# Performance work log

Hardware: AMD Instinct MI355X
Metric: run time of the kernel (lower is better)

## Reference

```python
import jax, jax.numpy as jnp
from jax import lax
import numpy as np

STEP = 0.01
BS = 32  # blocksize


def conv(x, w, b=None, stride=1, pad=0):
    y = lax.conv_general_dilated(x, w, (stride, stride), [(pad, pad), (pad, pad)],
                                 dimension_numbers=('NCHW', 'OIHW', 'NCHW'))
    if b is not None:
        y = y + b[None, :, None, None]
    return y


def prelu(x, a):
    return jnp.where(x >= 0, x, a * x)


def depth_to_space(x, bs):
    # matches Reshape_Concat_Adap: each [C] pixel vector viewed as (C', bs, bs)
    B, C, h, w = x.shape
    C2 = C // (bs * bs)
    y = x.reshape(B, C2, bs, bs, h, w)
    y = y.transpose(0, 1, 4, 2, 5, 3)  # B, C2, h, bs, w, bs
    return y.reshape(B, C2, h * bs, w * bs)


def setup_inputs() -> dict:
    key = jax.random.key(0)
    ks = jax.random.split(key, 32)

    def W(k, shape):
        fan_in = shape[1] * shape[2] * shape[3]
        return (jax.random.normal(k, shape, jnp.float32) * np.sqrt(2.0 / fan_in)).astype(jnp.float32)

    inp = {
        'x': jax.random.normal(ks[0], (4, 1, 192, 192), jnp.float32),
        'epoch': 1,
        'd1_w': W(ks[1], (16, 1, 4, 4)),
        'd2_w': W(ks[2], (256, 16, 4, 4)),
        'd3_w': W(ks[3], (1024, 256, 2, 2)),
        'd4_w': W(ks[4], (154, 1024, 1, 1)),
        'q1_w': W(ks[5], (154, 154, 1, 1)), 'q1_b': jnp.zeros((154,), jnp.float32),
        'q2_w': W(ks[6], (154, 154, 1, 1)), 'q2_b': jnp.zeros((154,), jnp.float32),
        'q3_w': W(ks[7], (154, 154, 1, 1)), 'q3_b': jnp.zeros((154,), jnp.float32),
        'up_w': W(ks[8], (1024, 154, 1, 1)), 'up_b': jnp.zeros((1024,), jnp.float32),
        'c1_w': W(ks[9], (64, 1, 3, 3)), 'c1_b': jnp.zeros((64,), jnp.float32), 'c1_a': jnp.float32(0.25),
        'c2_w': W(ks[10], (64, 64, 3, 3)), 'c2_b': jnp.zeros((64,), jnp.float32), 'c2_a': jnp.float32(0.25),
        'c3_w': W(ks[11], (64, 64, 3, 3)), 'c3_b': jnp.zeros((64,), jnp.float32), 'c3_a': jnp.float32(0.25),
        'c4_w': W(ks[12], (64, 64, 3, 3)), 'c4_b': jnp.zeros((64,), jnp.float32), 'c4_a': jnp.float32(0.25),
        'c5_w': W(ks[13], (256, 64, 3, 3)), 'c5_b': jnp.zeros((256,), jnp.float32),
    }
    return inp


def reference(x, epoch, d1_w, d2_w, d3_w, d4_w, q1_w, q1_b, q2_w, q2_b, q3_w, q3_b,
              up_w, up_b, c1_w, c1_b, c1_a, c2_w, c2_b, c2_a, c3_w, c3_b, c3_a,
              c4_w, c4_b, c4_a, c5_w, c5_b):
    step = jnp.float32(STEP)
    relu = jax.nn.relu
    # down path
    h = relu(conv(x, d1_w, stride=4))
    h = relu(conv(h, d2_w, stride=4))
    h = relu(conv(h, d3_w, stride=2))
    x4 = conv(h, d4_w)                      # [B,154,H/32,W/32]
    # STE quantize + dequantize
    q = x4 + lax.stop_gradient(jnp.floor(x4 / step) - x4)
    xr = q * step
    t = xr
    t = relu(conv(t, q1_w, q1_b)) + t
    t = relu(conv(t, q2_w, q2_b)) + t
    t = relu(conv(t, q3_w, q3_b)) + t
    x_comp = t + xr
    # upsample to blocksize^2 channels, then depth-to-space
    u = conv(x_comp, up_w, up_b)            # [B,1024,H/32,W/32]
    y = depth_to_space(u, BS)               # [B,1,H,W]
    # refinement CNN
    b1 = prelu(conv(y, c1_w, c1_b, pad=1), c1_a)
    b2 = prelu(conv(b1 + y, c2_w, c2_b, pad=1), c2_a)
    b3 = prelu(conv(b2 + b1, c3_w, c3_b, pad=1), c3_a)
    b4 = prelu(conv(b3 + b2, c4_w, c4_b, pad=1), c4_a)
    b5 = conv(b4 + b3, c5_w, c5_b, pad=1)   # [B,256,H,W]
    B, _, H, Wd = b5.shape
    return (b5.reshape(B, 1, 256, H, Wd), x_comp, x4)
```

## Files before the change

### kernel.cpp

```cpp
#include <hip/hip_runtime.h>
#include <math.h>

#define N_B 4
#define IMG 192
#define P 194

typedef __attribute__((ext_vector_type(8))) short short8;
typedef __attribute__((ext_vector_type(4))) float f32x4;

__device__ __forceinline__ unsigned f2bf(float f) {
  unsigned u = __float_as_uint(f);
  return (u + 0x7fffu + ((u >> 16) & 1u)) >> 16;
}
__device__ __forceinline__ float bf2f(unsigned b) {
  return __uint_as_float(b << 16);
}
__device__ __forceinline__ int swz(int pix) {
  return (pix & 7) << 4;
}
__device__ __forceinline__ void gload_lds16(const void* g, void* l) {
  __builtin_amdgcn_global_load_lds(
      (const __attribute__((address_space(1))) void*)g,
      (__attribute__((address_space(3))) void*)l, 16, 0, 0);
}

__global__ void k_d1(const float* __restrict__ x, const float* __restrict__ w,
                     float* __restrict__ out) {
  int idx = blockIdx.x * 256 + threadIdx.x;
  if (idx >= N_B * 16 * 48 * 48) return;
  int xq = idx % 48; int t = idx / 48; int yq = t % 48; t /= 48;
  int oc = t % 16; int b = t / 16;
  const float* xp = x + (b * IMG + yq * 4) * IMG + xq * 4;
  const float* wp = w + oc * 16;
  float s = 0.f;
#pragma unroll
  for (int dy = 0; dy < 4; ++dy)
#pragma unroll
    for (int dx = 0; dx < 4; ++dx)
      s = fmaf(xp[dy * IMG + dx], wp[dy * 4 + dx], s);
  out[idx] = fmaxf(s, 0.f);
}

__global__ void k_d2(const float* __restrict__ h1, const float* __restrict__ d2t,
                     float* __restrict__ out) {
  int idx = blockIdx.x * 256 + threadIdx.x;
  if (idx >= N_B * 144 * 256) return;
  int oc = idx & 255; int t = idx >> 8; int p = t % 144; int b = t / 144;
  int yq = p / 12, xq = p % 12;
  float s = 0.f;
  for (int ci = 0; ci < 16; ++ci) {
    const float* ip = h1 + ((b * 16 + ci) * 48 + yq * 4) * 48 + xq * 4;
    const float* wp = d2t + (ci * 16) * 256 + oc;
#pragma unroll
    for (int dy = 0; dy < 4; ++dy)
#pragma unroll
      for (int dx = 0; dx < 4; ++dx)
        s = fmaf(ip[dy * 48 + dx], wp[(dy * 4 + dx) * 256], s);
  }
  out[((size_t)b * 144 + p) * 256 + oc] = fmaxf(s, 0.f);
}

__global__ __launch_bounds__(256) void k_d3(const float* __restrict__ h2t,
                                            const float* __restrict__ w3p,
                                            float* __restrict__ out) {
  int idx = blockIdx.x * 256 + threadIdx.x;
  if (idx >= N_B * 36 * 1024) return;
  int oc = idx & 1023; int t = idx >> 10; int p6 = t % 36; int b = t / 36;
  int yq = p6 / 6, xq = p6 % 6;
  const float* p00 = h2t + ((size_t)b * 144 + (2 * yq) * 12 + 2 * xq) * 256;
  const float* p01 = p00 + 256;
  const float* p10 = p00 + 12 * 256;
  const float* p11 = p10 + 256;
  const float* w0 = w3p + oc;
  float a0 = 0.f, a1 = 0.f, a2 = 0.f, a3 = 0.f;
  for (int ci = 0; ci < 256; ++ci) {
    a0 = fmaf(p00[ci], w0[(size_t)(0 * 256 + ci) * 1024], a0);
    a1 = fmaf(p01[ci], w0[(size_t)(1 * 256 + ci) * 1024], a1);
    a2 = fmaf(p10[ci], w0[(size_t)(2 * 256 + ci) * 1024], a2);
    a3 = fmaf(p11[ci], w0[(size_t)(3 * 256 + ci) * 1024], a3);
  }
  out[((size_t)b * 36 + p6) * 1024 + oc] = fmaxf((a0 + a1) + (a2 + a3), 0.f);
}

__global__ __launch_bounds__(512) void k_mid(
    const float* __restrict__ h3t, const float* __restrict__ d4t,
    const float* __restrict__ qt, const float* __restrict__ q1_b,
    const float* __restrict__ q2_b, const float* __restrict__ q3_b,
    const float* __restrict__ upt, const float* __restrict__ up_b,
    float* __restrict__ x4_out, float* __restrict__ xcomp_out,
    float* __restrict__ y_out) {
  __shared__ float hv[1024];
  __shared__ float part[512];
  __shared__ float tv[160];
  __shared__ float xrv[160];
  int blk = blockIdx.x;
  int b = blk / 36, p = blk % 36;
  int tid = threadIdx.x;
  for (int i = tid; i < 1024; i += 512) hv[i] = h3t[(size_t)blk * 1024 + i];
  __syncthreads();
  {
    int half = tid >> 8, oc = tid & 255;
    float s = 0.f;
    if (oc < 154) {
      const float* wp = d4t + (size_t)half * 512 * 160 + oc;
      const float* hp = hv + half * 512;
      float a0 = 0.f, a1 = 0.f, a2 = 0.f, a3 = 0.f;
      for (int i = 0; i < 512; i += 4) {
        a0 = fmaf(hp[i], wp[(size_t)i * 160], a0);
        a1 = fmaf(hp[i + 1], wp[(size_t)(i + 1) * 160], a1);
        a2 = fmaf(hp[i + 2], wp[(size_t)(i + 2) * 160], a2);
        a3 = fmaf(hp[i + 3], wp[(size_t)(i + 3) * 160], a3);
      }
      s = (a0 + a1) + (a2 + a3);
    }
    part[tid] = s;
  }
  __syncthreads();
  if (tid < 154) {
    float s = part[tid] + part[tid + 256];
    x4_out[(b * 154 + tid) * 36 + p] = s;
    float q = floorf(s / 0.01f) * 0.01f;
    xrv[tid] = q;
    tv[tid] = q;
  }
  __syncthreads();
  const float* qb[3] = {q1_b, q2_b, q3_b};
  for (int l = 0; l < 3; ++l) {
    float s = 0.f;
    if (tid < 154) {
      const float* wp = qt + (size_t)l * 154 * 160 + tid;
      float a0 = 0.f, a1 = 0.f;
      int i = 0;
      for (; i + 1 < 154; i += 2) {
        a0 = fmaf(tv[i], wp[(size_t)i * 160], a0);
        a1 = fmaf(tv[i + 1], wp[(size_t)(i + 1) * 160], a1);
      }
      if (i < 154) a0 = fmaf(tv[i], wp[(size_t)i * 160], a0);
      s = qb[l][tid] + a0 + a1;
    }
    __syncthreads();
    if (tid < 154) tv[tid] = fmaxf(s, 0.f) + tv[tid];
    __syncthreads();
  }
  if (tid < 154) {
    float xc = tv[tid] + xrv[tid];
    tv[tid] = xc;
    xcomp_out[(b * 154 + tid) * 36 + p] = xc;
  }
  __syncthreads();
  int h = p / 6, w6 = p % 6;
#pragma unroll
  for (int k = 0; k < 2; ++k) {
    int co = k * 512 + tid;
    const float* wp = upt + co;
    float a0 = 0.f, a1 = 0.f;
    int i = 0;
    for (; i + 1 < 154; i += 2) {
      a0 = fmaf(tv[i], wp[(size_t)i * 1024], a0);
      a1 = fmaf(tv[i + 1], wp[(size_t)(i + 1) * 1024], a1);
    }
    if (i < 154) a0 = fmaf(tv[i], wp[(size_t)i * 1024], a0);
    float s = up_b[co] + a0 + a1;
    int i32 = co >> 5, j = co & 31;
    y_out[(b * IMG + h * 32 + i32) * IMG + w6 * 32 + j] = s;
  }
}

__global__ __launch_bounds__(256) void k_c1b(const float* __restrict__ y,
                                             const float* __restrict__ w,
                                             const float* __restrict__ bias,
                                             const float* __restrict__ a_p,
                                             short* __restrict__ B1,
                                             short* __restrict__ S1) {
  int idx = blockIdx.x * 256 + threadIdx.x;
  if (idx >= N_B * IMG * IMG) return;
  int X = idx % IMG; int t = idx / IMG; int Y = t % IMG; int b = t / IMG;
  float p[9];
#pragma unroll
  for (int dy = 0; dy < 3; ++dy)
#pragma unroll
    for (int dx = 0; dx < 3; ++dx) {
      int gy = Y + dy - 1, gx = X + dx - 1;
      p[dy * 3 + dx] = ((unsigned)gy < (unsigned)IMG && (unsigned)gx < (unsigned)IMG)
                           ? y[(b * IMG + gy) * IMG + gx]
                           : 0.f;
    }
  float a = *a_p;
  float yc = p[4];
  size_t base = (((size_t)b * P + Y + 1) * P + X + 1) * 64;
  for (int oc = 0; oc < 64; oc += 8) {
    unsigned bw[4], sw[4];
#pragma unroll
    for (int j = 0; j < 8; ++j) {
      float s = bias[oc + j];
      const float* wq = w + (oc + j) * 9;
#pragma unroll
      for (int k = 0; k < 9; ++k) s = fmaf(p[k], wq[k], s);
      s = s >= 0.f ? s : a * s;
      float sv = s + yc;
      if (j & 1) { bw[j >> 1] |= f2bf(s) << 16; sw[j >> 1] |= f2bf(sv) << 16; }
      else       { bw[j >> 1] = f2bf(s);        sw[j >> 1] = f2bf(sv); }
    }
    *(uint4*)(B1 + base + oc) = make_uint4(bw[0], bw[1], bw[2], bw[3]);
    *(uint4*)(S1 + base + oc) = make_uint4(sw[0], sw[1], sw[2], sw[3]);
  }
}

#define WPA (64 * 64 * 9)
#define WPB (256 * 64 * 9)
#define WD3N (4 * 256 * 1024)
#define RINGN (4 * 4 * 772 * 8)
#define D4TN (1024 * 154)
#define QTN (3 * 154 * 154)
#define UPTN (154 * 1024)
#define D2TN (256 * 16 * 16)
#define PREPN (3 * WPA + WPB + WD3N + RINGN + D4TN + QTN + UPTN + D2TN)
__global__ __launch_bounds__(256) void k_prep(
    const float* __restrict__ w2, const float* __restrict__ w3,
    const float* __restrict__ w4, const float* __restrict__ w5,
    const float* __restrict__ d3w, const float* __restrict__ d4w,
    const float* __restrict__ q1w, const float* __restrict__ q2w,
    const float* __restrict__ q3w, const float* __restrict__ upw,
    const float* __restrict__ d2w,
    short* __restrict__ o2, short* __restrict__ o3,
    short* __restrict__ o4, short* __restrict__ o5,
    float* __restrict__ w3p, float* __restrict__ d4t,
    float* __restrict__ qt, float* __restrict__ upt,
    float* __restrict__ d2t,
    short* __restrict__ s0, short* __restrict__ s1,
    short* __restrict__ s2, short* __restrict__ s3) {
  int idx = blockIdx.x * 256 + threadIdx.x;
  if (idx < 3 * WPA + WPB) {
    int which, id;
    if (idx < WPA) { which = 0; id = idx; }
    else if (idx < 2 * WPA) { which = 1; id = idx - WPA; }
    else if (idx < 3 * WPA) { which = 2; id = idx - 2 * WPA; }
    else { which = 3; id = idx - 3 * WPA; }
    const float* w = (which == 0) ? w2 : (which == 1) ? w3 : (which == 2) ? w4 : w5;
    short* o = (which == 0) ? o2 : (which == 1) ? o3 : (which == 2) ? o4 : o5;
    int OC = (which == 3) ? 256 : 64;
    int ic = id & 63; int t = id >> 6; int r = t % OC; int tap = t / OC;
    int oc = (which < 3) ? (((r >> 2) & 3) * 16 + ((r >> 4) & 3) * 4 + (r & 3)) : r;
    int ks = ic >> 5, lg = (ic >> 3) & 3, j = ic & 7, li = r & 15, ocblk = r >> 4;
    size_t dst = ((size_t)(tap * 2 + ks) * (OC >> 4) + ocblk) * 512 +
                 (lg * 16 + li) * 8 + j;
    o[dst] = (short)f2bf(w[((size_t)oc * 64 + ic) * 9 + tap]);
    return;
  }
  idx -= 3 * WPA + WPB;
  if (idx < WD3N) {
    int oc = idx & 1023; int ci = (idx >> 10) & 255; int tap = idx >> 18;
    w3p[idx] = d3w[((size_t)oc * 256 + ci) * 4 + tap];
    return;
  }
  idx -= WD3N;
  if (idx < RINGN) {
    int chunk = idx & 7; int t = idx >> 3;
    int r = t % 772; t /= 772; int b = t % 4; int buf = t / 4;
    int y, x;
    if (r < 194) { y = 0; x = r; }
    else if (r < 388) { y = 193; x = r - 194; }
    else { int q = r - 388; y = 1 + (q >> 1); x = (q & 1) ? 193 : 0; }
    short* p = (buf == 0) ? s0 : (buf == 1) ? s1 : (buf == 2) ? s2 : s3;
    *(uint4*)(p + (((size_t)b * P + y) * P + x) * 64 + chunk * 8) =
        make_uint4(0u, 0u, 0u, 0u);
    return;
  }
  idx -= RINGN;
  if (idx < D4TN) {
    int oc = idx % 154; int ic = idx / 154;
    d4t[(size_t)ic * 160 + oc] = d4w[(size_t)oc * 1024 + ic];
    return;
  }
  idx -= D4TN;
  if (idx < QTN) {
    int l = idx / (154 * 154); int rem = idx % (154 * 154);
    int oc = rem % 154; int ic = rem / 154;
    const float* qw = (l == 0) ? q1w : (l == 1) ? q2w : q3w;
    qt[(size_t)l * 154 * 160 + (size_t)ic * 160 + oc] =
        qw[(size_t)oc * 154 + ic];
    return;
  }
  idx -= QTN;
  if (idx < UPTN) {
    int co = idx % 1024; int ic = idx / 1024;
    upt[(size_t)ic * 1024 + co] = upw[(size_t)co * 154 + ic];
    return;
  }
  idx -= UPTN;
  if (idx < D2TN) {
    int oc = idx & 255; int t = idx >> 8; int tap = t & 15; int ci = t >> 4;
    d2t[((size_t)ci * 16 + tap) * 256 + oc] =
        d2w[((size_t)oc * 16 + ci) * 16 + tap];
  }
}

template <int MODE>
__global__ __launch_bounds__(256) void k_conv3x3n(
    const short* __restrict__ sin, const short* __restrict__ bprev,
    const short* __restrict__ wbf, const float* __restrict__ bias,
    const float* __restrict__ a_p, short* __restrict__ bout,
    short* __restrict__ sout) {
  __shared__ __align__(16) char smem[300 * 128];
  int tid = threadIdx.x;
  int b = blockIdx.z;
  int x0 = blockIdx.x * 48, y0 = blockIdx.y * 4;
  int w = tid >> 6, lane = tid & 63, li = lane & 15, lg = lane >> 4;

  for (int c = w; c < 38; c += 4) {
    int o = c * 1024 + lane * 16;
    if (o < 300 * 128) {
      int pix = o >> 7;
      int icq = ((o >> 4) & 7) ^ (pix & 7);
      const short* src = sin +
          (((size_t)b * P + y0 + pix / 50) * P + x0 + pix % 50) * 64 + icq * 8;
      gload_lds16(src, smem + c * 1024);
    }
  }
  __syncthreads();

  const short* abase = wbf + (lane << 3);
  const int astride = 64 * 32;

  f32x4 acc[4][3];
#pragma unroll
  for (int mt = 0; mt < 4; ++mt)
#pragma unroll
    for (int nt = 0; nt < 3; ++nt) acc[mt][nt] = (f32x4){0.f, 0.f, 0.f, 0.f};

#define LOADA(s, dst)                                                          \
  {                                                                            \
    const short* p_ = abase + (size_t)(s) * astride;                           \
    _Pragma("unroll") for (int mt = 0; mt < 4; ++mt)                           \
        dst[mt] = *(const short8*)(p_ + mt * 512);                             \
  }
#define LOADB(s, dst)                                                          \
  {                                                                            \
    const int tap_ = (s) >> 1, ks_ = (s) & 1;                                  \
    const int dy_ = tap_ / 3, dx_ = tap_ % 3;                                  \
    _Pragma("unroll") for (int nt = 0; nt < 3; ++nt) {                         \
      int pix_ = (w + dy_) * 50 + nt * 16 + dx_ + li;                          \
      int byte_ = (pix_ * 128 + ks_ * 64 + lg * 16) ^ swz(pix_);               \
      dst[nt] = *(const short8*)(smem + byte_);                                \
    }                                                                          \
  }

  short8 Abuf[2][4];
  short8 Bbuf[3];
  LOADA(0, Abuf[0]);
#pragma unroll
  for (int s = 0; s < 18; ++s) {
    if (s + 1 < 18) LOADA(s + 1, Abuf[(s + 1) & 1]);
    LOADB(s, Bbuf);
    short8* Ac = Abuf[s & 1];
#pragma unroll
    for (int mt = 0; mt < 4; ++mt)
#pragma unroll
      for (int nt = 0; nt < 3; ++nt)
        acc[mt][nt] = __builtin_amdgcn_mfma_f32_16x16x32_bf16(Ac[mt], Bbuf[nt],
                                                              acc[mt][nt], 0, 0, 0);
  }
#undef LOADA
#undef LOADB

  float a = *a_p;
  int gy = y0 + w;
#pragma unroll
  for (int nt = 0; nt < 3; ++nt) {
    int gx = x0 + nt * 16 + li;
    float r[16];
#pragma unroll
    for (int mt = 0; mt < 4; ++mt) {
      float4 bv = *(const float4*)(bias + lg * 16 + mt * 4);
      f32x4 v = acc[mt][nt];
      float t0 = v[0] + bv.x, t1 = v[1] + bv.y, t2 = v[2] + bv.z, t3 = v[3] + bv.w;
      r[mt * 4 + 0] = t0 >= 0.f ? t0 : a * t0;
      r[mt * 4 + 1] = t1 >= 0.f ? t1 : a * t1;
      r[mt * 4 + 2] = t2 >= 0.f ? t2 : a * t2;
      r[mt * 4 + 3] = t3 >= 0.f ? t3 : a * t3;
    }
    size_t pi = (((size_t)b * P + gy + 1) * P + gx + 1) * 64 + lg * 16;
    if (MODE == 0) {
      uint4 u0 = make_uint4(f2bf(r[0]) | (f2bf(r[1]) << 16),
                            f2bf(r[2]) | (f2bf(r[3]) << 16),
                            f2bf(r[4]) | (f2bf(r[5]) << 16),
                            f2bf(r[6]) | (f2bf(r[7]) << 16));
      uint4 u1 = make_uint4(f2bf(r[8]) | (f2bf(r[9]) << 16),
                            f2bf(r[10]) | (f2bf(r[11]) << 16),
                            f2bf(r[12]) | (f2bf(r[13]) << 16),
                            f2bf(r[14]) | (f2bf(r[15]) << 16));
      *(uint4*)(bout + pi) = u0;
      *(uint4*)(bout + pi + 8) = u1;
    }
    uint4 p0 = *(const uint4*)(bprev + pi);
    uint4 p1 = *(const uint4*)(bprev + pi + 8);
    unsigned pw[8] = {p0.x, p0.y, p0.z, p0.w, p1.x, p1.y, p1.z, p1.w};
    unsigned so[8];
#pragma unroll
    for (int k = 0; k < 8; ++k) {
      float s0 = r[2 * k] + bf2f(pw[k] & 0xffffu);
      float s1 = r[2 * k + 1] + bf2f(pw[k] >> 16);
      so[k] = f2bf(s0) | (f2bf(s1) << 16);
    }
    *(uint4*)(sout + pi) = make_uint4(so[0], so[1], so[2], so[3]);
    *(uint4*)(sout + pi + 8) = make_uint4(so[4], so[5], so[6], so[7]);
  }
}

__global__ __launch_bounds__(256) void k_conv5n(
    const short* __restrict__ sin, const short* __restrict__ wbf,
    const float* __restrict__ bias, float* __restrict__ fout) {
  __shared__ __align__(16) char smem[300 * 128];
  int tid = threadIdx.x;
  int g = blockIdx.z & 3, b = blockIdx.z >> 2;
  int x0 = blockIdx.x * 48, y0 = blockIdx.y * 4;
  int w = tid >> 6, lane = tid & 63, li = lane & 15, lg = lane >> 4;

  for (int c = w; c < 38; c += 4) {
    int o = c * 1024 + lane * 16;
    if (o < 300 * 128) {
      int pix = o >> 7;
      int icq = ((o >> 4) & 7) ^ (pix & 7);
      const short* src = sin +
          (((size_t)b * P + y0 + pix / 50) * P + x0 + pix % 50) * 64 + icq * 8;
      gload_lds16(src, smem + c * 1024);
    }
  }
  __syncthreads();

  const short* abase = wbf + (size_t)(g << 2) * 512 + (lane << 3);
  const int astride = 256 * 32;

  f32x4 acc[4][3];
#pragma unroll
  for (int mt = 0; mt < 4; ++mt)
#pragma unroll
    for (int nt = 0; nt < 3; ++nt) acc[mt][nt] = (f32x4){0.f, 0.f, 0.f, 0.f};

#define LOADA5(s, dst)                                                         \
  {                                                                            \
    const short* p_ = abase + (size_t)(s) * astride;                           \
    _Pragma("unroll") for (int mt = 0; mt < 4; ++mt)                           \
        dst[mt] = *(const short8*)(p_ + mt * 512);                             \
  }
#define LOADB5(s, dst)                                                         \
  {                                                                            \
    const int tap_ = (s) >> 1, ks_ = (s) & 1;                                  \
    const int dy_ = tap_ / 3, dx_ = tap_ % 3;                                  \
    _Pragma("unroll") for (int nt = 0; nt < 3; ++nt) {                         \
      int pix_ = (w + dy_) * 50 + nt * 16 + dx_ + li;                          \
      int byte_ = (pix_ * 128 + ks_ * 64 + lg * 16) ^ swz(pix_);               \
      dst[nt] = *(const short8*)(smem + byte_);                                \
    }                                                                          \
  }

  short8 Abuf[2][4];
  short8 Bbuf[3];
  LOADA5(0, Abuf[0]);
#pragma unroll
  for (int s = 0; s < 18; ++s) {
    if (s + 1 < 18) LOADA5(s + 1, Abuf[(s + 1) & 1]);
    LOADB5(s, Bbuf);
    short8* Ac = Abuf[s & 1];
#pragma unroll
    for (int mt = 0; mt < 4; ++mt)
#pragma unroll
      for (int nt = 0; nt < 3; ++nt)
        acc[mt][nt] = __builtin_amdgcn_mfma_f32_16x16x32_bf16(Bbuf[nt], Ac[mt],
                                                              acc[mt][nt], 0, 0, 0);
  }
#undef LOADA5
#undef LOADB5

  int gy = y0 + w;
#pragma unroll
  for (int nt = 0; nt < 3; ++nt) {
    int gx = x0 + nt * 16 + lg * 4;
#pragma unroll
    for (int mt = 0; mt < 4; ++mt) {
      int oc = g * 64 + mt * 16 + li;
      float bv = bias[oc];
      f32x4 v = acc[mt][nt];
      *(float4*)(fout + (((size_t)b * 256 + oc) * IMG + gy) * IMG + gx) =
          make_float4(v[0] + bv, v[1] + bv, v[2] + bv, v[3] + bv);
    }
  }
}

extern "C" void kernel_launch(void* const* d_in, const int* in_sizes, int n_in,
                              void* d_out, int out_size, void* d_ws, size_t ws_size,
                              hipStream_t stream) {
  const float* x    = (const float*)d_in[0];
  const float* d1_w = (const float*)d_in[2];
  const float* d2_w = (const float*)d_in[3];
  const float* d3_w = (const float*)d_in[4];
  const float* d4_w = (const float*)d_in[5];
  const float* q1_w = (const float*)d_in[6];
  const float* q1_b = (const float*)d_in[7];
  const float* q2_w = (const float*)d_in[8];
  const float* q2_b = (const float*)d_in[9];
  const float* q3_w = (const float*)d_in[10];
  const float* q3_b = (const float*)d_in[11];
  const float* up_w = (const float*)d_in[12];
  const float* up_b = (const float*)d_in[13];
  const float* c1_w = (const float*)d_in[14];
  const float* c1_b = (const float*)d_in[15];
  const float* c1_a = (const float*)d_in[16];
  const float* c2_w = (const float*)d_in[17];
  const float* c2_b = (const float*)d_in[18];
  const float* c2_a = (const float*)d_in[19];
  const float* c3_w = (const float*)d_in[20];
  const float* c3_b = (const float*)d_in[21];
  const float* c3_a = (const float*)d_in[22];
  const float* c4_w = (const float*)d_in[23];
  const float* c4_b = (const float*)d_in[24];
  const float* c4_a = (const float*)d_in[25];
  const float* c5_w = (const float*)d_in[26];
  const float* c5_b = (const float*)d_in[27];

  float* out = (float*)d_out;
  float* ws  = (float*)d_ws;

  const size_t B5  = (size_t)N_B * 256 * IMG * IMG;
  const size_t SML = (size_t)N_B * 154 * 36;
  float* out_b5    = out;
  float* out_xcomp = out + B5;
  float* out_x4    = out + B5 + SML;

  const size_t PADBUF = (size_t)N_B * P * P * 64 / 2;
  size_t off = 0;
  float* h1   = ws + off; off += (size_t)N_B * 16 * 48 * 48;
  float* h2t  = ws + off; off += (size_t)N_B * 144 * 256;
  float* h3t  = ws + off; off += (size_t)N_B * 36 * 1024;
  float* w3p  = ws + off; off += (size_t)4 * 256 * 1024;
  float* d4t  = ws + off; off += (size_t)1024 * 160;
  float* qt   = ws + off; off += (size_t)3 * 154 * 160;
  float* upt  = ws + off; off += (size_t)154 * 1024;
  float* d2t  = ws + off; off += (size_t)256 * 16 * 16;
  float* ybuf = ws + off; off += (size_t)N_B * IMG * IMG;
  short* sl0  = (short*)(ws + off); off += PADBUF;
  short* sl1  = (short*)(ws + off); off += PADBUF;
  short* sl2  = (short*)(ws + off); off += PADBUF;
  short* sl3  = (short*)(ws + off); off += PADBUF;
  short* wb2  = (short*)(ws + off); off += 9 * 64 * 64 / 2;
  short* wb3  = (short*)(ws + off); off += 9 * 64 * 64 / 2;
  short* wb4  = (short*)(ws + off); off += 9 * 64 * 64 / 2;
  short* wb5  = (short*)(ws + off); off += 9 * 256 * 64 / 2;

  k_prep<<<(PREPN + 255) / 256, 256, 0, stream>>>(
      c2_w, c3_w, c4_w, c5_w, d3_w, d4_w, q1_w, q2_w, q3_w, up_w, d2_w,
      wb2, wb3, wb4, wb5, w3p, d4t, qt, upt, d2t, sl0, sl1, sl2, sl3);

  k_d1<<<(N_B * 16 * 48 * 48 + 255) / 256, 256, 0, stream>>>(x, d1_w, h1);
  k_d2<<<(N_B * 144 * 256 + 255) / 256, 256, 0, stream>>>(h1, d2t, h2t);
  k_d3<<<(N_B * 36 * 1024 + 255) / 256, 256, 0, stream>>>(h2t, w3p, h3t);

  k_mid<<<N_B * 36, 512, 0, stream>>>(h3t, d4t, qt, q1_b, q2_b, q3_b,
                                      upt, up_b, out_x4, out_xcomp, ybuf);

  k_c1b<<<(N_B * IMG * IMG + 255) / 256, 256, 0, stream>>>(ybuf, c1_w, c1_b, c1_a,
                                                           sl1 , sl0 );

  dim3 cg(4, 48, N_B);
  k_conv3x3n<0><<<cg, 256, 0, stream>>>(sl0, sl1, wb2, c2_b, c2_a, sl2, sl3);
  k_conv3x3n<0><<<cg, 256, 0, stream>>>(sl3, sl2, wb3, c3_b, c3_a, sl1, sl0);
  k_conv3x3n<1><<<cg, 256, 0, stream>>>(sl0, sl1, wb4, c4_b, c4_a, nullptr, sl3);
  dim3 cg5(4, 48, N_B * 4);
  k_conv5n<<<cg5, 256, 0, stream>>>(sl3, wb5, c5_b, out_b5);
}
```

Baseline: 285.3 us.

## Register-block d3 over four pixels and reuse conv5 input tile across two OC groups

k_d3 now computes four output pixels per thread, so each weight load is reused four times, and the grid shrinks to 144 blocks. The w3p prep loop is rewritten to read d3w sequentially and scatter writes, giving coalesced reads instead of coalesced writes. k_conv5n processes two 64-channel output groups per block, so the LDS input tile is loaded once for 128 channels and the grid halves. The cost is fewer blocks, which lowers parallelism, and each conv5 block now runs two sequential MFMA passes.

```diff
diff --git a/kernel.cpp b/kernel.cpp
--- a/kernel.cpp
+++ b/kernel.cpp
@@ -63,23 +63,39 @@
 __global__ __launch_bounds__(256) void k_d3(const float* __restrict__ h2t,
                                             const float* __restrict__ w3p,
                                             float* __restrict__ out) {
-  int idx = blockIdx.x * 256 + threadIdx.x;
-  if (idx >= N_B * 36 * 1024) return;
-  int oc = idx & 1023; int t = idx >> 10; int p6 = t % 36; int b = t / 36;
-  int yq = p6 / 6, xq = p6 % 6;
-  const float* p00 = h2t + ((size_t)b * 144 + (2 * yq) * 12 + 2 * xq) * 256;
-  const float* p01 = p00 + 256;
-  const float* p10 = p00 + 12 * 256;
-  const float* p11 = p10 + 256;
+  int tid = threadIdx.x;
+  int blk = blockIdx.x;
+  int og = blk & 3; int t = blk >> 2; int pg = t % 9; int b = t / 9;
+  int oc = og * 256 + tid;
   const float* w0 = w3p + oc;
-  float a0 = 0.f, a1 = 0.f, a2 = 0.f, a3 = 0.f;
+  const float* base[4];
+#pragma unroll
+  for (int k = 0; k < 4; ++k) {
+    int p6 = pg * 4 + k;
+    int yq = p6 / 6, xq = p6 % 6;
+    base[k] = h2t + ((size_t)b * 144 + (2 * yq) * 12 + 2 * xq) * 256;
+  }
+  float a0[4] = {0, 0, 0, 0}, a1[4] = {0, 0, 0, 0};
+  float a2[4] = {0, 0, 0, 0}, a3[4] = {0, 0, 0, 0};
   for (int ci = 0; ci < 256; ++ci) {
-    a0 = fmaf(p00[ci], w0[(size_t)(0 * 256 + ci) * 1024], a0);
-    a1 = fmaf(p01[ci], w0[(size_t)(1 * 256 + ci) * 1024], a1);
-    a2 = fmaf(p10[ci], w0[(size_t)(2 * 256 + ci) * 1024], a2);
-    a3 = fmaf(p11[ci], w0[(size_t)(3 * 256 + ci) * 1024], a3);
-  }
-  out[((size_t)b * 36 + p6) * 1024 + oc] = fmaxf((a0 + a1) + (a2 + a3), 0.f);
+    float w0v = w0[(size_t)(0 * 256 + ci) * 1024];
+    float w1v = w0[(size_t)(1 * 256 + ci) * 1024];
+    float w2v = w0[(size_t)(2 * 256 + ci) * 1024];
+    float w3v = w0[(size_t)(3 * 256 + ci) * 1024];
+#pragma unroll
+    for (int k = 0; k < 4; ++k) {
+      a0[k] = fmaf(base[k][ci], w0v, a0[k]);
+      a1[k] = fmaf(base[k][256 + ci], w1v, a1[k]);
+      a2[k] = fmaf(base[k][12 * 256 + ci], w2v, a2[k]);
+      a3[k] = fmaf(base[k][12 * 256 + 256 + ci], w3v, a3[k]);
+    }
+  }
+#pragma unroll
+  for (int k = 0; k < 4; ++k) {
+    int p6 = pg * 4 + k;
+    out[((size_t)b * 36 + p6) * 1024 + oc] =
+        fmaxf((a0[k] + a1[k]) + (a2[k] + a3[k]), 0.f);
+  }
 }
 
 __global__ __launch_bounds__(512) void k_mid(
@@ -249,8 +265,8 @@
   }
   idx -= 3 * WPA + WPB;
   if (idx < WD3N) {
-    int oc = idx & 1023; int ci = (idx >> 10) & 255; int tap = idx >> 18;
-    w3p[idx] = d3w[((size_t)oc * 256 + ci) * 4 + tap];
+    int tap = idx & 3; int ci = (idx >> 2) & 255; int oc = idx >> 10;
+    w3p[((size_t)tap * 256 + ci) * 1024 + oc] = d3w[idx];
     return;
   }
   idx -= WD3N;
@@ -412,7 +428,7 @@
     const float* __restrict__ bias, float* __restrict__ fout) {
   __shared__ __align__(16) char smem[300 * 128];
   int tid = threadIdx.x;
-  int g = blockIdx.z & 3, b = blockIdx.z >> 2;
+  int gh = blockIdx.z & 1, b = blockIdx.z >> 1;
   int x0 = blockIdx.x * 48, y0 = blockIdx.y * 4;
   int w = tid >> 6, lane = tid & 63, li = lane & 15, lg = lane >> 4;
 
@@ -428,18 +444,12 @@
   }
   __syncthreads();
 
-  const short* abase = wbf + (size_t)(g << 2) * 512 + (lane << 3);
   const int astride = 256 * 32;
-
-  f32x4 acc[4][3];
-#pragma unroll
-  for (int mt = 0; mt < 4; ++mt)
-#pragma unroll
-    for (int nt = 0; nt < 3; ++nt) acc[mt][nt] = (f32x4){0.f, 0.f, 0.f, 0.f};
-
-#define LOADA5(s, dst)                                                         \
+  int gy = y0 + w;
+
+#define LOADA5(s, dst, ab)                                                     \
   {                                                                            \
-    const short* p_ = abase + (size_t)(s) * astride;                           \
+    const short* p_ = (ab) + (size_t)(s) * astride;                            \
     _Pragma("unroll") for (int mt = 0; mt < 4; ++mt)                           \
         dst[mt] = *(const short8*)(p_ + mt * 512);                             \
   }
@@ -454,37 +464,48 @@
     }                                                                          \
   }
 
-  short8 Abuf[2][4];
-  short8 Bbuf[3];
-  LOADA5(0, Abuf[0]);
-#pragma unroll
-  for (int s = 0; s < 18; ++s) {
-    if (s + 1 < 18) LOADA5(s + 1, Abuf[(s + 1) & 1]);
-    LOADB5(s, Bbuf);
-    short8* Ac = Abuf[s & 1];
+#pragma unroll
+  for (int gg = 0; gg < 2; ++gg) {
+    const int g = gh * 2 + gg;
+    const short* abase = wbf + (size_t)(g << 2) * 512 + (lane << 3);
+
+    f32x4 acc[4][3];
 #pragma unroll
     for (int mt = 0; mt < 4; ++mt)
 #pragma unroll
-      for (int nt = 0; nt < 3; ++nt)
-        acc[mt][nt] = __builtin_amdgcn_mfma_f32_16x16x32_bf16(Bbuf[nt], Ac[mt],
-                                                              acc[mt][nt], 0, 0, 0);
+      for (int nt = 0; nt < 3; ++nt) acc[mt][nt] = (f32x4){0.f, 0.f, 0.f, 0.f};
+
+    short8 Abuf[2][4];
+    short8 Bbuf[3];
+    LOADA5(0, Abuf[0], abase);
+#pragma unroll
+    for (int s = 0; s < 18; ++s) {
+      if (s + 1 < 18) LOADA5(s + 1, Abuf[(s + 1) & 1], abase);
+      LOADB5(s, Bbuf);
+      short8* Ac = Abuf[s & 1];
+#pragma unroll
+      for (int mt = 0; mt < 4; ++mt)
+#pragma unroll
+        for (int nt = 0; nt < 3; ++nt)
+          acc[mt][nt] = __builtin_amdgcn_mfma_f32_16x16x32_bf16(
+              Bbuf[nt], Ac[mt], acc[mt][nt], 0, 0, 0);
+    }
+
+#pragma unroll
+    for (int nt = 0; nt < 3; ++nt) {
+      int gx = x0 + nt * 16 + lg * 4;
+#pragma unroll
+      for (int mt = 0; mt < 4; ++mt) {
+        int oc = g * 64 + mt * 16 + li;
+        float bv = bias[oc];
+        f32x4 v = acc[mt][nt];
+        *(float4*)(fout + (((size_t)b * 256 + oc) * IMG + gy) * IMG + gx) =
+            make_float4(v[0] + bv, v[1] + bv, v[2] + bv, v[3] + bv);
+      }
+    }
   }
 #undef LOADA5
 #undef LOADB5
-
-  int gy = y0 + w;
-#pragma unroll
-  for (int nt = 0; nt < 3; ++nt) {
-    int gx = x0 + nt * 16 + lg * 4;
-#pragma unroll
-    for (int mt = 0; mt < 4; ++mt) {
-      int oc = g * 64 + mt * 16 + li;
-      float bv = bias[oc];
-      f32x4 v = acc[mt][nt];
-      *(float4*)(fout + (((size_t)b * 256 + oc) * IMG + gy) * IMG + gx) =
-          make_float4(v[0] + bv, v[1] + bv, v[2] + bv, v[3] + bv);
-    }
-  }
 }
 
 extern "C" void kernel_launch(void* const* d_in, const int* in_sizes, int n_in,
@@ -553,7 +574,7 @@
 
   k_d1<<<(N_B * 16 * 48 * 48 + 255) / 256, 256, 0, stream>>>(x, d1_w, h1);
   k_d2<<<(N_B * 144 * 256 + 255) / 256, 256, 0, stream>>>(h1, d2t, h2t);
-  k_d3<<<(N_B * 36 * 1024 + 255) / 256, 256, 0, stream>>>(h2t, w3p, h3t);
+  k_d3<<<144, 256, 0, stream>>>(h2t, w3p, h3t);
 
   k_mid<<<N_B * 36, 512, 0, stream>>>(h3t, d4t, qt, q1_b, q2_b, q3_b,
                                       upt, up_b, out_x4, out_xcomp, ybuf);
@@ -565,6 +586,6 @@
   k_conv3x3n<0><<<cg, 256, 0, stream>>>(sl0, sl1, wb2, c2_b, c2_a, sl2, sl3);
   k_conv3x3n<0><<<cg, 256, 0, stream>>>(sl3, sl2, wb3, c3_b, c3_a, sl1, sl0);
   k_conv3x3n<1><<<cg, 256, 0, stream>>>(sl0, sl1, wb4, c4_b, c4_a, nullptr, sl3);
-  dim3 cg5(4, 48, N_B * 4);
+  dim3 cg5(4, 48, N_B * 2);
   k_conv5n<<<cg5, 256, 0, stream>>>(sl3, wb5, c5_b, out_b5);
 }
```

Measured after the change: 291.5 us. 2.2% more time.
